# Optimization experiments

Measured on AMD Instinct MI355X. Metric: run time of the kernel, lower is better.

The kernel has to match this reference:

```python
import jax, jax.numpy as jnp
import numpy as np

# Geometry from the hard-coded `options` tensor
VIEWS, DETS = 160, 640
H, W = 416, 416
D_IMG = 0.006641            # image pixel size
D_DET = 0.012858            # detector bin size
ANG0 = 0.0
D_ANG = 0.009817477 * 4     # = 2*pi/160 (full scan)
S2R = 5.95                  # source-to-rotation-center distance
D2R = 4.906                 # detector-to-rotation-center distance
VIRDET = D_DET * S2R / (S2R + D2R)   # detector rescaled to isocenter (virtual detector)
PI = float(np.pi)
COEF = PI / VIEWS
BATCH = 32


def setup_inputs() -> dict:
    key = jax.random.key(0)
    projection = jax.random.normal(key, (BATCH, 1, VIEWS, DETS), dtype=jnp.float32)

    # Ramp filter (Ram-Lak, spatial domain), length 2*dets-1, exactly as in torch __init__
    x = np.arange(2 * DETS - 1) - DETS + 1
    x_safe = np.where(x == 0, 1, x).astype(np.float64)
    filt = np.where(np.abs(x) % 2 == 1,
                    -1.0 / (PI * PI * x_safe * x_safe * VIRDET * VIRDET),
                    0.0)
    filt[x == 0] = 1.0 / (4.0 * VIRDET * VIRDET)
    filt = jnp.asarray(filt.reshape(1, 1, 1, -1), dtype=jnp.float32)

    # Cosine (fan-beam) pre-weighting, detector bin centers at (i - dets/2 + 0.5)*virdet
    u = (np.arange(DETS) - DETS / 2 + 0.5) * VIRDET
    wv = S2R / np.sqrt(S2R ** 2 + u ** 2) * VIRDET
    w = jnp.asarray(wv.reshape(1, 1, 1, -1), dtype=jnp.float32)

    return {"projection": projection, "w": w, "filt": filt}


def _backproject(p):
    """Pixel-driven equidistant fan-beam backprojection.
    p: filtered sinogram [B, 1, VIEWS, DETS] -> recon [B, 1, H, W].
    """
    betas = ANG0 + D_ANG * jnp.arange(VIEWS, dtype=jnp.float32)
    xs = (jnp.arange(W, dtype=jnp.float32) - (W - 1) / 2.0) * D_IMG   # [W]
    ys = ((H - 1) / 2.0 - jnp.arange(H, dtype=jnp.float32)) * D_IMG   # [H]
    Xg, Yg = jnp.meshgrid(xs, ys)   # both [H, W]

    pv = jnp.moveaxis(p, 2, 0)  # [VIEWS, B, 1, DETS]

    def step(acc, inp):
        beta, pb = inp                      # pb: [B, 1, DETS]
        cb, sb = jnp.cos(beta), jnp.sin(beta)
        d = Xg * cb + Yg * sb               # pixel component toward source
        r = -Xg * sb + Yg * cb              # perpendicular component
        U = S2R - d                         # source-to-pixel depth
        # detector coordinate at isocenter -> fractional bin index
        idx = (S2R * r / U) / VIRDET + (DETS - 1) / 2.0   # [H, W]
        valid = (idx >= 0.0) & (idx <= DETS - 1)
        i0 = jnp.clip(jnp.floor(idx), 0, DETS - 2).astype(jnp.int32)
        frac = jnp.clip(idx - i0.astype(jnp.float32), 0.0, 1.0)
        # irregular gather + linear interpolation: [B,1,H,W]
        v = pb[:, :, i0] * (1.0 - frac) + pb[:, :, i0 + 1] * frac
        wgt = jnp.where(valid, (S2R / U) ** 2, 0.0)       # distance weighting
        return acc + wgt * v, None

    init = jnp.zeros((p.shape[0], 1, H, W), dtype=p.dtype)
    acc, _ = jax.lax.scan(step, init, (betas, pv))
    return acc


def reference(projection, w, filt):
    # 1) cosine weighting (elementwise broadcast over detector axis)
    p = projection * w
    p = jax.lax.conv_general_dilated(
        p, filt, window_strides=(1, 1),
        padding=((0, 0), (DETS - 1, DETS - 1)),
        dimension_numbers=("NCHW", "OIHW", "NCHW"))
    # 3) geometric backprojection + angular step normalization
    return COEF * _backproject(p)
```

## Files before the change

### kernel.cpp

```cpp
#include <hip/hip_runtime.h>

#define VIEWS 160
#define DETS  640
#define H_IMG 416
#define W_IMG 416
#define BATCH 32

constexpr double D_IMG_D  = 0.006641;
constexpr double D_DET_D  = 0.012858;
constexpr double S2R_D    = 5.95;
constexpr double D2R_D    = 4.906;
constexpr double VIRDET_D = D_DET_D * S2R_D / (S2R_D + D2R_D);
constexpr double PI_D     = 3.14159265358979323846;

typedef __fp16 __attribute__((ext_vector_type(2))) h2f;

#define TILES_X 13
#define TILES_Y 52
#define NTILES  (TILES_X * TILES_Y)
#define NB      64
#define ZSPLIT  3
#define OUT_F4  ((size_t)BATCH * H_IMG * W_IMG / 4)


__device__ __forceinline__ float dot2_asm(unsigned int p, unsigned int w, float c) {
    float d;
    asm("v_dot2_f32_f16 %0, %1, %2, %3" : "=v"(d) : "v"(p), "v"(w), "v"(c));
    return d;
}

#define FT 320
#define RPAD 24
#define RSTR 209
__global__ __launch_bounds__(FT) void filter_kernel(
    const float* __restrict__ proj, const float* __restrict__ w,
    const float* __restrict__ filt, unsigned int* __restrict__ pf3,
    float* __restrict__ vcs, int* __restrict__ bs_tab,
    float4* __restrict__ out4) {
    __shared__ float4 s_in[4 * RSTR];
    __shared__ float  s_f[2 * DETS];
    __shared__ unsigned int s_out[2 * DETS];

    int t = threadIdx.x;
    int g = blockIdx.x;
    int group4 = g / 160;
    int v = g - group4 * 160;

    {
        float dang = (float)(0.009817477 * 4.0);
        float K    = (float)(S2R_D / VIRDET_D);
        if (g == 0 && t < VIEWS) {
            float beta = dang * (float)t;
            float cb = cosf(beta), sb = sinf(beta);
            ((float4*)vcs)[t] = make_float4(cb, sb, -K * sb, K * cb);
        }
        int e = g * 85 + t;
        if (t < 85 && e < NTILES * VIEWS) {
            int tile = e / 160;
            int vv   = e - tile * 160;
            float beta = dang * (float)vv;
            float cb = cosf(beta), sb = sinf(beta);
            int ty = tile / TILES_X, tx = tile - ty * TILES_X;
            float XL = ((float)(tx * 32) - 207.5f) * (float)D_IMG_D;
            float XR = ((float)(tx * 32 + 31) - 207.5f) * (float)D_IMG_D;
            float YT = (207.5f - (float)(ty * 8)) * (float)D_IMG_D;
            float YB = (207.5f - (float)(ty * 8 + 7)) * (float)D_IMG_D;
            float m = 1e30f;
#define CORNER(Xc, Yc) { \
            float r_ = -(Xc) * sb + (Yc) * cb; \
            float U_ = (float)S2R_D - (Xc) * cb - (Yc) * sb; \
            float ix = fmaf(K, r_ / U_, 319.5f); \
            m = fminf(m, ix); }
            CORNER(XL, YT); CORNER(XR, YT); CORNER(XL, YB); CORNER(XR, YB);
#undef CORNER
            int bs = (int)floorf(m) - 2;
            bs = max(0, min(DETS - NB, bs)) & ~1;
            bs_tab[e] = bs;
        }
        float4 z = make_float4(0.f, 0.f, 0.f, 0.f);
        for (int i = t; i < 1082; i += FT) {
            size_t o = (size_t)g * 1082 + i;
            if (o < OUT_F4) out4[o] = z;
        }
    }

    for (int e = t; e < 4 * RSTR; e += FT) {
        int ri = e / RSTR, c4 = e - ri * RSTR;
        float4 pv = make_float4(0.f, 0.f, 0.f, 0.f);
        if (c4 >= RPAD && c4 < RPAD + 160) {
            int b = group4 * 4 + ri;
            pv = ((const float4*)(proj + ((size_t)b * VIEWS + v) * DETS))[c4 - RPAD];
            float4 wv = ((const float4*)w)[c4 - RPAD];
            pv.x *= wv.x; pv.y *= wv.y; pv.z *= wv.z; pv.w *= wv.w;
        }
        s_in[e] = pv;
    }
    for (int e = t; e < 2 * DETS; e += FT) s_f[e] = (e < 2 * DETS - 1) ? filt[e] : 0.f;
    __syncthreads();

    int sub = (t >= 160) ? 1 : 0;
    int tj  = t - sub * 160;

    const float4* f4  = (const float4*)s_f;
    const float4* in4 = &s_in[sub * 2 * RSTR + tj];
    float4 o0 = {0,0,0,0}, o1 = {0,0,0,0};
    float4 fp = f4[135];
    #pragma unroll 2
    for (int u = 0; u < 50; ++u) {
        float4 fn = f4[136 + u];
        {
            float4 iv = in4[0 * RSTR + u];
            o0.x = fmaf(iv.x, fp.w, o0.x); o0.x = fmaf(iv.y, fn.x, o0.x);
            o0.x = fmaf(iv.z, fn.y, o0.x); o0.x = fmaf(iv.w, fn.z, o0.x);
            o0.y = fmaf(iv.x, fp.z, o0.y); o0.y = fmaf(iv.y, fp.w, o0.y);
            o0.y = fmaf(iv.z, fn.x, o0.y); o0.y = fmaf(iv.w, fn.y, o0.y);
            o0.z = fmaf(iv.x, fp.y, o0.z); o0.z = fmaf(iv.y, fp.z, o0.z);
            o0.z = fmaf(iv.z, fp.w, o0.z); o0.z = fmaf(iv.w, fn.x, o0.z);
            o0.w = fmaf(iv.x, fp.x, o0.w); o0.w = fmaf(iv.y, fp.y, o0.w);
            o0.w = fmaf(iv.z, fp.z, o0.w); o0.w = fmaf(iv.w, fp.w, o0.w);
        }
        {
            float4 iv = in4[1 * RSTR + u];
            o1.x = fmaf(iv.x, fp.w, o1.x); o1.x = fmaf(iv.y, fn.x, o1.x);
            o1.x = fmaf(iv.z, fn.y, o1.x); o1.x = fmaf(iv.w, fn.z, o1.x);
            o1.y = fmaf(iv.x, fp.z, o1.y); o1.y = fmaf(iv.y, fp.w, o1.y);
            o1.y = fmaf(iv.z, fn.x, o1.y); o1.y = fmaf(iv.w, fn.y, o1.y);
            o1.z = fmaf(iv.x, fp.y, o1.z); o1.z = fmaf(iv.y, fp.z, o1.z);
            o1.z = fmaf(iv.z, fp.w, o1.z); o1.z = fmaf(iv.w, fn.x, o1.z);
            o1.w = fmaf(iv.x, fp.x, o1.w); o1.w = fmaf(iv.y, fp.y, o1.w);
            o1.w = fmaf(iv.z, fp.z, o1.w); o1.w = fmaf(iv.w, fp.w, o1.w);
        }
        fp = fn;
    }

    float coef = (float)((PI_D / (double)VIEWS) * S2R_D * S2R_D);
    auto h0 = __builtin_amdgcn_cvt_pkrtz(o0.x * coef, o1.x * coef);
    auto h1 = __builtin_amdgcn_cvt_pkrtz(o0.y * coef, o1.y * coef);
    auto h2 = __builtin_amdgcn_cvt_pkrtz(o0.z * coef, o1.z * coef);
    auto h3 = __builtin_amdgcn_cvt_pkrtz(o0.w * coef, o1.w * coef);
    uint4 pk = make_uint4(__builtin_bit_cast(unsigned int, h0),
                          __builtin_bit_cast(unsigned int, h1),
                          __builtin_bit_cast(unsigned int, h2),
                          __builtin_bit_cast(unsigned int, h3));
    *(uint4*)&s_out[sub * DETS + 4 * tj] = pk;
    __syncthreads();

    unsigned int* dstv = pf3 + (size_t)v * 20480 + (size_t)group4 * 4;
    #pragma unroll
    for (int cc = 0; cc < 2; ++cc) {
        int j  = 2 * t + cc;
        int j1 = j + 1;
        unsigned int u0  = s_out[j];
        unsigned int u0n = (j1 < DETS) ? s_out[j1] : 0u;
        unsigned int u1  = s_out[DETS + j];
        unsigned int u1n = (j1 < DETS) ? s_out[DETS + j1] : 0u;
        uint4 o;
        o.x = __builtin_amdgcn_perm(u0n, u0, 0x05040100u);
        o.y = __builtin_amdgcn_perm(u0n, u0, 0x07060302u);
        o.z = __builtin_amdgcn_perm(u1n, u1, 0x05040100u);
        o.w = __builtin_amdgcn_perm(u1n, u1, 0x07060302u);
        *(uint4*)(dstv + (size_t)j * 32) = o;
    }
}

__device__ __forceinline__ void gld_lds16(const char* g, char* l) {
    __builtin_amdgcn_global_load_lds(
        (const __attribute__((address_space(1))) unsigned int*)g,
        (__attribute__((address_space(3))) unsigned int*)l, 16, 0, 0);
}

__global__ __launch_bounds__(256, 8) void bp_kernel(
    const unsigned int* __restrict__ pf3, const float* __restrict__ vcs,
    const int* __restrict__ bs_tab, float* __restrict__ out) {
    __shared__ alignas(16) unsigned int s_buf[2 * 2048];

    int t    = threadIdx.x;
    int zc   = blockIdx.z;
    int tile = blockIdx.y * TILES_X + blockIdx.x;
    int xl   = ((t >> 6) << 3) + (t & 7);
    int yl   = (t >> 3) & 7;
    int x    = blockIdx.x * 32 + xl;
    int y    = blockIdx.y * 8 + yl;

    float X  = ((float)x - 207.5f) * (float)D_IMG_D;
    float Yv = (207.5f - (float)y) * (float)D_IMG_D;

    int vstart = (zc * VIEWS) / ZSPLIT;
    int vend   = ((zc + 1) * VIEWS) / ZSPLIT;
    int nv     = vend - vstart;
    const float4* vc4 = (const float4*)vcs + vstart;
    const int*    bsp = bs_tab + tile * VIEWS + vstart;
    const char*   pfb = (const char*)pf3 + (size_t)vstart * 81920;

    int r_s  = (t >> 3) & 31;
    int k_s  = t & 7;
    int toff0 = r_s * 128 + ((k_s ^ (r_s & 7)) << 4);
    int wvbase = (t >> 6) << 10;

    float acc[32];
    #pragma unroll
    for (int b = 0; b < 32; ++b) acc[b] = 0.f;

    #define STAGE(c) do { \
        int bsd = bsp[(c)]; \
        const char* src = pfb + (size_t)(c) * 81920 + (size_t)bsd * 128 + toff0; \
        char* dst = (char*)s_buf + (((c) & 1) << 13) + wvbase; \
        gld_lds16(src, dst); \
        gld_lds16(src + 4096, dst + 4096); \
    } while (0)

    #define GEOM(a_, bs_, w01_, b2r_) do { \
        float U    = fmaf(-X, (a_).x, fmaf(-Yv, (a_).y, (float)S2R_D)); \
        float num  = fmaf(X, (a_).z, Yv * (a_).w); \
        float ru   = __builtin_amdgcn_rcpf(U); \
        float idx  = fmaf(num, ru, 319.5f); \
        float idxc = __builtin_amdgcn_fmed3f(idx, 0.f, 639.f); \
        float i0f  = fminf(idxc, 638.0f); \
        int   i0   = (int)i0f; \
        float frac = idxc - truncf(i0f); \
        float w2   = ru * ru; \
        float wgt  = (idx == idxc) ? w2 : 0.f; \
        float w1f  = wgt * frac; \
        float w0f  = wgt - w1f; \
        w01_ = __builtin_bit_cast(unsigned int, __builtin_amdgcn_cvt_pkrtz(w0f, w1f)); \
        int rel = min(max(i0 - (bs_), 0), NB - 2); \
        b2r_ = (rel << 7) + ((rel & 7) << 4); \
    } while (0)

    STAGE(0);
    unsigned int w01_cur; int b2r_cur;
    {   float4 a0 = vc4[0]; GEOM(a0, bsp[0], w01_cur, b2r_cur); }
    __syncthreads();

    for (int c = 0; c < nv; ++c) {
        if (c + 1 < nv) STAGE(c + 1);

        const char* pbase = (const char*)s_buf + ((c & 1) << 13);
        int b2  = b2r_cur;
        unsigned int w01 = w01_cur;
        uint4 q0 = *(const uint4*)(pbase + (b2 ^ 0));
        uint4 q1 = *(const uint4*)(pbase + (b2 ^ 16));
        uint4 q2 = *(const uint4*)(pbase + (b2 ^ 32));
        uint4 q3 = *(const uint4*)(pbase + (b2 ^ 48));

        if (c + 1 < nv) {
            float4 an = vc4[c + 1];
            GEOM(an, bsp[c + 1], w01_cur, b2r_cur);
        }

        acc[0]  = dot2_asm(q0.x, w01, acc[0]);
        acc[1]  = dot2_asm(q0.y, w01, acc[1]);
        acc[2]  = dot2_asm(q0.z, w01, acc[2]);
        acc[3]  = dot2_asm(q0.w, w01, acc[3]);
        acc[4]  = dot2_asm(q1.x, w01, acc[4]);
        acc[5]  = dot2_asm(q1.y, w01, acc[5]);
        acc[6]  = dot2_asm(q1.z, w01, acc[6]);
        acc[7]  = dot2_asm(q1.w, w01, acc[7]);

        uint4 q4 = *(const uint4*)(pbase + (b2 ^ 64));
        uint4 q5 = *(const uint4*)(pbase + (b2 ^ 80));
        uint4 q6 = *(const uint4*)(pbase + (b2 ^ 96));
        uint4 q7 = *(const uint4*)(pbase + (b2 ^ 112));

        acc[8]  = dot2_asm(q2.x, w01, acc[8]);
        acc[9]  = dot2_asm(q2.y, w01, acc[9]);
        acc[10] = dot2_asm(q2.z, w01, acc[10]);
        acc[11] = dot2_asm(q2.w, w01, acc[11]);
        acc[12] = dot2_asm(q3.x, w01, acc[12]);
        acc[13] = dot2_asm(q3.y, w01, acc[13]);
        acc[14] = dot2_asm(q3.z, w01, acc[14]);
        acc[15] = dot2_asm(q3.w, w01, acc[15]);
        acc[16] = dot2_asm(q4.x, w01, acc[16]);
        acc[17] = dot2_asm(q4.y, w01, acc[17]);
        acc[18] = dot2_asm(q4.z, w01, acc[18]);
        acc[19] = dot2_asm(q4.w, w01, acc[19]);
        acc[20] = dot2_asm(q5.x, w01, acc[20]);
        acc[21] = dot2_asm(q5.y, w01, acc[21]);
        acc[22] = dot2_asm(q5.z, w01, acc[22]);
        acc[23] = dot2_asm(q5.w, w01, acc[23]);
        acc[24] = dot2_asm(q6.x, w01, acc[24]);
        acc[25] = dot2_asm(q6.y, w01, acc[25]);
        acc[26] = dot2_asm(q6.z, w01, acc[26]);
        acc[27] = dot2_asm(q6.w, w01, acc[27]);
        acc[28] = dot2_asm(q7.x, w01, acc[28]);
        acc[29] = dot2_asm(q7.y, w01, acc[29]);
        acc[30] = dot2_asm(q7.z, w01, acc[30]);
        acc[31] = dot2_asm(q7.w, w01, acc[31]);

        __syncthreads();
    }
    #undef STAGE
    #undef GEOM

    float* s_t = (float*)s_buf;
    int px    = yl * 32 + xl;
    int swz_w = px ^ ((yl & 3) << 3);
    int swz_r = t  ^ (((t >> 5) & 3) << 3);
    float* ob = out + (size_t)(blockIdx.y * 8 + (t >> 5)) * W_IMG
                    + blockIdx.x * 32 + (t & 31);
    #pragma unroll
    for (int p = 0; p < 2; ++p) {
        __syncthreads();
        #pragma unroll
        for (int bi = 0; bi < 16; ++bi)
            s_t[bi * 256 + swz_w] = acc[p * 16 + bi];
        __syncthreads();
        #pragma unroll
        for (int bi = 0; bi < 16; ++bi)
            unsafeAtomicAdd(ob + (size_t)(p * 16 + bi) * (H_IMG * W_IMG),
                            s_t[bi * 256 + swz_r]);
    }
}

extern "C" void kernel_launch(void* const* d_in, const int* in_sizes, int n_in,
                              void* d_out, int out_size, void* d_ws, size_t ws_size,
                              hipStream_t stream) {
    const float* proj = (const float*)d_in[0];
    const float* w    = (const float*)d_in[1];
    const float* filt = (const float*)d_in[2];
    float* out = (float*)d_out;

    float*        vcs    = (float*)d_ws;
    int*          bs_tab = (int*)((char*)d_ws + 4096);
    unsigned int* pf3    = (unsigned int*)((char*)d_ws + 442368);

    filter_kernel<<<(BATCH / 4) * VIEWS, FT, 0, stream>>>(proj, w, filt, pf3,
                                                          vcs, bs_tab, (float4*)out);
    bp_kernel<<<dim3(TILES_X, TILES_Y, ZSPLIT), 256, 0, stream>>>(pf3, vcs, bs_tab, out);
}
```

Baseline: 188.1 us.

## Exploit Ram-Lak zero even taps via even/odd polyphase split in filter

The ramp filter convolution is rewritten to use the fact that the Ram-Lak kernel is nonzero only at odd offsets plus the center tap. Input detector samples are split into even and odd phases so each output phase convolves only the opposite phase with the odd taps, plus a separate center-tap term. The filter is truncated to about 103 odd taps around the center, the same window length the old loop used. The cost being removed is the roughly half of the FMAs that multiplied by zero taps, along with some shared-memory traffic; the price is a more intricate index layout and a reshuffled pack/store epilogue.

```diff
diff --git a/kernel.cpp b/kernel.cpp
--- a/kernel.cpp
+++ b/kernel.cpp
@@ -30,16 +30,14 @@
 }
 
 #define FT 320
-#define RPAD 24
-#define RSTR 209
 __global__ __launch_bounds__(FT) void filter_kernel(
     const float* __restrict__ proj, const float* __restrict__ w,
     const float* __restrict__ filt, unsigned int* __restrict__ pf3,
     float* __restrict__ vcs, int* __restrict__ bs_tab,
     float4* __restrict__ out4) {
-    __shared__ float4 s_in[4 * RSTR];
-    __shared__ float  s_f[2 * DETS];
-    __shared__ unsigned int s_out[2 * DETS];
+    __shared__ float4 s_par[8 * 106];
+    __shared__ float  s_fo[112];
+    __shared__ unsigned int s_res[4 * 320];
 
     int t = threadIdx.x;
     int g = blockIdx.x;
@@ -84,83 +82,85 @@
         }
     }
 
-    for (int e = t; e < 4 * RSTR; e += FT) {
-        int ri = e / RSTR, c4 = e - ri * RSTR;
-        float4 pv = make_float4(0.f, 0.f, 0.f, 0.f);
-        if (c4 >= RPAD && c4 < RPAD + 160) {
-            int b = group4 * 4 + ri;
-            pv = ((const float4*)(proj + ((size_t)b * VIEWS + v) * DETS))[c4 - RPAD];
-            float4 wv = ((const float4*)w)[c4 - RPAD];
-            pv.x *= wv.x; pv.y *= wv.y; pv.z *= wv.z; pv.w *= wv.w;
-        }
-        s_in[e] = pv;
-    }
-    for (int e = t; e < 2 * DETS; e += FT) s_f[e] = (e < 2 * DETS - 1) ? filt[e] : 0.f;
+    {
+        float4 z = make_float4(0.f, 0.f, 0.f, 0.f);
+        for (int i = t; i < 8 * 106; i += FT) s_par[i] = z;
+        if (t < 112) s_fo[t] = (t >= 6 && t <= 108) ? filt[528 + 2 * t] : 0.f;
+    }
     __syncthreads();
 
-    int sub = (t >= 160) ? 1 : 0;
-    int tj  = t - sub * 160;
-
-    const float4* f4  = (const float4*)s_f;
-    const float4* in4 = &s_in[sub * 2 * RSTR + tj];
-    float4 o0 = {0,0,0,0}, o1 = {0,0,0,0};
-    float4 fp = f4[135];
-    #pragma unroll 2
-    for (int u = 0; u < 50; ++u) {
-        float4 fn = f4[136 + u];
-        {
-            float4 iv = in4[0 * RSTR + u];
-            o0.x = fmaf(iv.x, fp.w, o0.x); o0.x = fmaf(iv.y, fn.x, o0.x);
-            o0.x = fmaf(iv.z, fn.y, o0.x); o0.x = fmaf(iv.w, fn.z, o0.x);
-            o0.y = fmaf(iv.x, fp.z, o0.y); o0.y = fmaf(iv.y, fp.w, o0.y);
-            o0.y = fmaf(iv.z, fn.x, o0.y); o0.y = fmaf(iv.w, fn.y, o0.y);
-            o0.z = fmaf(iv.x, fp.y, o0.z); o0.z = fmaf(iv.y, fp.z, o0.z);
-            o0.z = fmaf(iv.z, fp.w, o0.z); o0.z = fmaf(iv.w, fn.x, o0.z);
-            o0.w = fmaf(iv.x, fp.x, o0.w); o0.w = fmaf(iv.y, fp.y, o0.w);
-            o0.w = fmaf(iv.z, fp.z, o0.w); o0.w = fmaf(iv.w, fp.w, o0.w);
-        }
-        {
-            float4 iv = in4[1 * RSTR + u];
-            o1.x = fmaf(iv.x, fp.w, o1.x); o1.x = fmaf(iv.y, fn.x, o1.x);
-            o1.x = fmaf(iv.z, fn.y, o1.x); o1.x = fmaf(iv.w, fn.z, o1.x);
-            o1.y = fmaf(iv.x, fp.z, o1.y); o1.y = fmaf(iv.y, fp.w, o1.y);
-            o1.y = fmaf(iv.z, fn.x, o1.y); o1.y = fmaf(iv.w, fn.y, o1.y);
-            o1.z = fmaf(iv.x, fp.y, o1.z); o1.z = fmaf(iv.y, fp.z, o1.z);
-            o1.z = fmaf(iv.z, fp.w, o1.z); o1.z = fmaf(iv.w, fn.x, o1.z);
-            o1.w = fmaf(iv.x, fp.x, o1.w); o1.w = fmaf(iv.y, fp.y, o1.w);
-            o1.w = fmaf(iv.z, fp.z, o1.w); o1.w = fmaf(iv.w, fp.w, o1.w);
-        }
+    int r  = t / 80;
+    int tj = t - r * 80;
+    {
+        const float4* pr = (const float4*)(proj +
+            ((size_t)(group4 * 4 + r) * VIEWS + v) * DETS);
+        const float4* wr = (const float4*)w;
+        float4 a  = pr[2 * tj],  b  = pr[2 * tj + 1];
+        float4 wa = wr[2 * tj],  wb = wr[2 * tj + 1];
+        float4 e4 = make_float4(a.x * wa.x, a.z * wa.z, b.x * wb.x, b.z * wb.z);
+        float4 o4 = make_float4(a.y * wa.y, a.w * wa.w, b.y * wb.y, b.w * wb.w);
+        s_par[(0 * 4 + r) * 106 + 13 + tj] = e4;
+        s_par[(1 * 4 + r) * 106 + 13 + tj] = o4;
+    }
+    __syncthreads();
+
+    const float4* fo4 = (const float4*)s_fo;
+    const float4* oE  = &s_par[(0 * 4 + r) * 106 + tj];
+    const float4* oO  = &s_par[(1 * 4 + r) * 106 + tj];
+    float4 ae = {0, 0, 0, 0}, ao = {0, 0, 0, 0};
+    float4 fp = fo4[0];
+    for (int i = 0; i < 27; ++i) {
+        float4 fn = fo4[i + 1];
+        float4 vO = oO[i];
+        float4 vE = oE[i];
+        ae.x = fmaf(vO.x, fn.x, ae.x); ae.x = fmaf(vO.y, fn.y, ae.x);
+        ae.x = fmaf(vO.z, fn.z, ae.x); ae.x = fmaf(vO.w, fn.w, ae.x);
+        ae.y = fmaf(vO.x, fp.w, ae.y); ae.y = fmaf(vO.y, fn.x, ae.y);
+        ae.y = fmaf(vO.z, fn.y, ae.y); ae.y = fmaf(vO.w, fn.z, ae.y);
+        ae.z = fmaf(vO.x, fp.z, ae.z); ae.z = fmaf(vO.y, fp.w, ae.z);
+        ae.z = fmaf(vO.z, fn.x, ae.z); ae.z = fmaf(vO.w, fn.y, ae.z);
+        ae.w = fmaf(vO.x, fp.y, ae.w); ae.w = fmaf(vO.y, fp.z, ae.w);
+        ae.w = fmaf(vO.z, fp.w, ae.w); ae.w = fmaf(vO.w, fn.x, ae.w);
+        ao.x = fmaf(vE.x, fp.w, ao.x); ao.x = fmaf(vE.y, fn.x, ao.x);
+        ao.x = fmaf(vE.z, fn.y, ao.x); ao.x = fmaf(vE.w, fn.z, ao.x);
+        ao.y = fmaf(vE.x, fp.z, ao.y); ao.y = fmaf(vE.y, fp.w, ao.y);
+        ao.y = fmaf(vE.z, fn.x, ao.y); ao.y = fmaf(vE.w, fn.y, ao.y);
+        ao.z = fmaf(vE.x, fp.y, ao.z); ao.z = fmaf(vE.y, fp.z, ao.z);
+        ao.z = fmaf(vE.z, fp.w, ao.z); ao.z = fmaf(vE.w, fn.x, ao.z);
+        ao.w = fmaf(vE.x, fp.x, ao.w); ao.w = fmaf(vE.y, fp.y, ao.w);
+        ao.w = fmaf(vE.z, fp.z, ao.w); ao.w = fmaf(vE.w, fp.w, ao.w);
         fp = fn;
     }
+    {
+        float c0 = filt[639];
+        float4 ce = oE[13], co = oO[13];
+        ae.x = fmaf(ce.x, c0, ae.x); ae.y = fmaf(ce.y, c0, ae.y);
+        ae.z = fmaf(ce.z, c0, ae.z); ae.w = fmaf(ce.w, c0, ae.w);
+        ao.x = fmaf(co.x, c0, ao.x); ao.y = fmaf(co.y, c0, ao.y);
+        ao.z = fmaf(co.z, c0, ao.z); ao.w = fmaf(co.w, c0, ao.w);
+    }
 
     float coef = (float)((PI_D / (double)VIEWS) * S2R_D * S2R_D);
-    auto h0 = __builtin_amdgcn_cvt_pkrtz(o0.x * coef, o1.x * coef);
-    auto h1 = __builtin_amdgcn_cvt_pkrtz(o0.y * coef, o1.y * coef);
-    auto h2 = __builtin_amdgcn_cvt_pkrtz(o0.z * coef, o1.z * coef);
-    auto h3 = __builtin_amdgcn_cvt_pkrtz(o0.w * coef, o1.w * coef);
-    uint4 pk = make_uint4(__builtin_bit_cast(unsigned int, h0),
-                          __builtin_bit_cast(unsigned int, h1),
-                          __builtin_bit_cast(unsigned int, h2),
-                          __builtin_bit_cast(unsigned int, h3));
-    *(uint4*)&s_out[sub * DETS + 4 * tj] = pk;
+    auto h0 = __builtin_amdgcn_cvt_pkrtz(ae.x * coef, ao.x * coef);
+    auto h1 = __builtin_amdgcn_cvt_pkrtz(ae.y * coef, ao.y * coef);
+    auto h2 = __builtin_amdgcn_cvt_pkrtz(ae.z * coef, ao.z * coef);
+    auto h3 = __builtin_amdgcn_cvt_pkrtz(ae.w * coef, ao.w * coef);
+    *(uint4*)&s_res[r * 320 + 4 * tj] = make_uint4(
+        __builtin_bit_cast(unsigned int, h0), __builtin_bit_cast(unsigned int, h1),
+        __builtin_bit_cast(unsigned int, h2), __builtin_bit_cast(unsigned int, h3));
     __syncthreads();
 
     unsigned int* dstv = pf3 + (size_t)v * 20480 + (size_t)group4 * 4;
-    #pragma unroll
-    for (int cc = 0; cc < 2; ++cc) {
-        int j  = 2 * t + cc;
-        int j1 = j + 1;
-        unsigned int u0  = s_out[j];
-        unsigned int u0n = (j1 < DETS) ? s_out[j1] : 0u;
-        unsigned int u1  = s_out[DETS + j];
-        unsigned int u1n = (j1 < DETS) ? s_out[DETS + j1] : 0u;
-        uint4 o;
-        o.x = __builtin_amdgcn_perm(u0n, u0, 0x05040100u);
-        o.y = __builtin_amdgcn_perm(u0n, u0, 0x07060302u);
-        o.z = __builtin_amdgcn_perm(u1n, u1, 0x05040100u);
-        o.w = __builtin_amdgcn_perm(u1n, u1, 0x07060302u);
-        *(uint4*)(dstv + (size_t)j * 32) = o;
-    }
+    unsigned int uA[4], uB[4];
+    for (int rr = 0; rr < 4; ++rr) {
+        unsigned int u  = s_res[rr * 320 + t];
+        unsigned int un = 0u;
+        if (t + 1 < 320) un = s_res[rr * 320 + t + 1];
+        uA[rr] = u;
+        uB[rr] = __builtin_amdgcn_perm(un, u, 0x05040302u);
+    }
+    *(uint4*)(dstv + (size_t)(2 * t) * 32)     = make_uint4(uA[0], uA[1], uA[2], uA[3]);
+    *(uint4*)(dstv + (size_t)(2 * t + 1) * 32) = make_uint4(uB[0], uB[1], uB[2], uB[3]);
 }
 
 __device__ __forceinline__ void gld_lds16(const char* g, char* l) {
```

Measured after the change: 185.5 us. About the same (-1.4%).
